# Optimization experiments

Measured on AMD Instinct MI355X. Metric: run time of the kernel, lower is better.

Reference implementation:

```python
import jax, jax.numpy as jnp
import numpy as np

B, H, W, C = 8, 64, 64, 768
NUM_HEADS = 12
KSIZE = 3
DILATIONS = (1, 2, 3)
ND = len(DILATIONS)
HEAD_DIM = C // NUM_HEADS  # 64
SCALE = HEAD_DIM ** (-0.5)


def setup_inputs() -> dict:
    key = jax.random.key(0)
    kx, kqkv, kpw, kpb = jax.random.split(key, 4)
    x = jax.random.normal(kx, (B, H, W, C), dtype=jnp.float32)
    # 1x1 conv qkv: weight [3C, C] (no bias, qkv_bias=False)
    qkv_w = jax.random.normal(kqkv, (3 * C, C), dtype=jnp.float32) * (C ** -0.5)
    # nn.Linear proj: weight [C, C], bias [C]
    proj_w = jax.random.normal(kpw, (C, C), dtype=jnp.float32) * (C ** -0.5)
    proj_b = jax.random.normal(kpb, (C,), dtype=jnp.float32) * 0.01
    return {"x": x, "qkv_w": qkv_w, "proj_w": proj_w, "proj_b": proj_b}


def _unfold(t, k, dil):
    # t: [B, d, H, W] -> [B, d, k*k, H, W]; matches nn.Unfold(k, dil, pad=dil*(k-1)//2)
    b, d, h, w = t.shape
    pad = dil * (k - 1) // 2
    tp = jnp.pad(t, ((0, 0), (0, 0), (pad, pad), (pad, pad)))
    patches = [tp[:, :, i * dil:i * dil + h, j * dil:j * dil + w]
               for i in range(k) for j in range(k)]
    return jnp.stack(patches, axis=2)


def reference(x, qkv_w, proj_w, proj_b):
    b, h, w, c = x.shape
    d = c // ND                 # channels per dilation group
    hpd = NUM_HEADS // ND       # heads per dilation group
    xc = x.transpose(0, 3, 1, 2)                      # [B, C, H, W]
    qkv = jnp.einsum('bchw,oc->bohw', xc, qkv_w)      # [B, 3C, H, W]
    qkv = qkv.reshape(b, 3, ND, d, h, w)
    outs = []
    for i, dil in enumerate(DILATIONS):
        q = qkv[:, 0, i].reshape(b, hpd, HEAD_DIM, h, w)
        ku = _unfold(qkv[:, 1, i], KSIZE, dil).reshape(b, hpd, HEAD_DIM, KSIZE * KSIZE, h, w)
        vu = _unfold(qkv[:, 2, i], KSIZE, dil).reshape(b, hpd, HEAD_DIM, KSIZE * KSIZE, h, w)
        attn = jnp.einsum('bnchw,bncKhw->bnKhw', q, ku) * SCALE
        attn = jax.nn.softmax(attn, axis=2)           # over the k*k neighborhood
        o = jnp.einsum('bnKhw,bncKhw->bnchw', attn, vu)  # [B, hpd, hd, H, W]
        outs.append(o.transpose(0, 3, 4, 1, 2).reshape(b, h, w, d))
    y = jnp.concatenate(outs, axis=-1)                # dilation-major channel order
    y = y + x                                          # DWConvAttention branch is identity
    y = jnp.einsum('bhwc,oc->bhwo', y, proj_w) + proj_b
    return y
```

## Files before the change

kernel.cpp:

```cpp
#include <hip/hip_runtime.h>
#include <hip/hip_bf16.h>

#define CC 768
#define MM 32768
#define NQKV 2304
#define SCALE_ 0.125f

typedef __bf16 bf16x8 __attribute__((ext_vector_type(8)));
typedef float f32x4 __attribute__((ext_vector_type(4)));
typedef unsigned short ushort8_t __attribute__((ext_vector_type(8)));

static __device__ __forceinline__ float bf2f(unsigned short u) {
  return __uint_as_float(((unsigned int)u) << 16);
}
static __device__ __forceinline__ unsigned short f2bf(float f) {
  __hip_bfloat16 t = __float2bfloat16(f);
  return __builtin_bit_cast(unsigned short, t);
}

__global__ void cvt_kernel(const float* __restrict__ in,
                           __hip_bfloat16* __restrict__ out, int n4) {
  int i = blockIdx.x * blockDim.x + threadIdx.x;
  if (i >= n4) return;
  float4 v = reinterpret_cast<const float4*>(in)[i];
  ushort4 o;
  o.x = f2bf(v.x); o.y = f2bf(v.y); o.z = f2bf(v.z); o.w = f2bf(v.w);
  reinterpret_cast<ushort4*>(out)[i] = o;
}

template <int MODE>
__global__ __launch_bounds__(256) void gemm_bf16_kernel(
    const __hip_bfloat16* __restrict__ A,
    const __hip_bfloat16* __restrict__ Bw,
    void* __restrict__ outp,
    const float* __restrict__ bias,
    int M, int N, int K) {
  __shared__ __hip_bfloat16 lA[3][128 * 32];
  __shared__ __hip_bfloat16 lB[3][128 * 32];

  const int nBN = N >> 7;
  const int cpx = gridDim.x >> 3;
  const int bid = ((int)blockIdx.x & 7) * cpx + ((int)blockIdx.x >> 3);
  const int bm = bid / nBN;
  const int bn = bid % nBN;
  const int tid = threadIdx.x;
  const int lane = tid & 63;
  const int wv = tid >> 6;
  const int wr = wv >> 1;
  const int wc = wv & 1;

  f32x4 acc[4][4] = {};

  const int srow = wv * 16 + (lane >> 2);
  const int scol = ((lane & 3) ^ ((lane >> 3) & 3)) * 8;
  const size_t Abase = (size_t)(bm * 128) * K;
  const size_t Bbase = (size_t)(bn * 128) * K;

  const int frow = lane & 15;
  const int g = lane >> 4;
  const int fcol = (g ^ ((frow >> 1) & 3)) * 8;

  auto stage = [&](int buf, int t) {
    const int k0 = t << 5;
#pragma unroll
    for (int c = 0; c < 2; ++c) {
      const __hip_bfloat16* gA = A + Abase + (size_t)(c * 64 + srow) * K + k0 + scol;
      __hip_bfloat16* sA = &lA[buf][(c * 64 + wv * 16) * 32];
      __builtin_amdgcn_global_load_lds(
          (const __attribute__((address_space(1))) void*)gA,
          (__attribute__((address_space(3))) void*)sA, 16, 0, 0);
      const __hip_bfloat16* gB = Bw + Bbase + (size_t)(c * 64 + srow) * K + k0 + scol;
      __hip_bfloat16* sB = &lB[buf][(c * 64 + wv * 16) * 32];
      __builtin_amdgcn_global_load_lds(
          (const __attribute__((address_space(1))) void*)gB,
          (__attribute__((address_space(3))) void*)sB, 16, 0, 0);
    }
  };

  const int nt = K >> 5;
  stage(0, 0);
  if (nt > 1) stage(1, 1);

  int rd = 0;
  int st = 2;
  for (int t = 0; t < nt; ++t) {
    if (t + 1 < nt) asm volatile("s_waitcnt vmcnt(4)" ::: "memory");
    else            asm volatile("s_waitcnt vmcnt(0)" ::: "memory");
    __builtin_amdgcn_s_barrier();
    asm volatile("" ::: "memory");

    bf16x8 af[4], bfr[4];
#pragma unroll
    for (int m = 0; m < 4; ++m)
      af[m] = *reinterpret_cast<const bf16x8*>(&lA[rd][(wr * 64 + m * 16 + frow) * 32 + fcol]);
#pragma unroll
    for (int n = 0; n < 4; ++n)
      bfr[n] = *reinterpret_cast<const bf16x8*>(&lB[rd][(wc * 64 + n * 16 + frow) * 32 + fcol]);

    if (t + 2 < nt) stage(st, t + 2);
#pragma unroll
    for (int m = 0; m < 4; ++m)
#pragma unroll
      for (int n = 0; n < 4; ++n)
        acc[m][n] = __builtin_amdgcn_mfma_f32_16x16x32_bf16(af[m], bfr[n], acc[m][n], 0, 0, 0);

    rd = (rd == 2) ? 0 : rd + 1;
    st = (st == 2) ? 0 : st + 1;
  }

  const int r0 = (lane >> 4) * 4;
  const int cc_ = lane & 15;
#pragma unroll
  for (int m = 0; m < 4; ++m) {
#pragma unroll
    for (int n = 0; n < 4; ++n) {
      const int grow = bm * 128 + wr * 64 + m * 16 + r0;
      const int gcol = bn * 128 + wc * 64 + n * 16 + cc_;
      if (MODE == 1) {
        __hip_bfloat16* outT = (__hip_bfloat16*)outp;
        ushort4 pk;
        pk.x = f2bf(acc[m][n][0]);
        pk.y = f2bf(acc[m][n][1]);
        pk.z = f2bf(acc[m][n][2]);
        pk.w = f2bf(acc[m][n][3]);
        *reinterpret_cast<ushort4*>(outT + (size_t)gcol * M + grow) = pk;
      } else {
        float* outF = (float*)outp;
        const float bv = bias ? bias[gcol] : 0.f;
#pragma unroll
        for (int r = 0; r < 4; ++r)
          outF[(size_t)(grow + r) * N + gcol] = acc[m][n][r] + bv;
      }
    }
  }
}

__global__ __launch_bounds__(256) void attn_kernel(
    const unsigned short* __restrict__ qkvT,
    const float* __restrict__ x,
    unsigned short* __restrict__ y) {
  const int head = blockIdx.x >> 7;
  const int p = ((blockIdx.x & 127) << 8) + threadIdx.x;
  const int h = (p >> 6) & 63;
  const int w = p & 63;
  const int grp = head >> 2;
  const int dil = grp + 1;
  const int chq = grp * 256 + (head & 3) * 64;

  int voff[9];
  bool valid[9];
#pragma unroll
  for (int t = 0; t < 9; ++t) {
    const int di = t / 3 - 1, dj = t % 3 - 1;
    valid[t] = ((unsigned)(h + di * dil) < 64u) && ((unsigned)(w + dj * dil) < 64u);
    voff[t] = p + (di * 64 + dj) * dil + 256;
  }
  const int voffq = p + 256;

  const unsigned short* qb = qkvT + (size_t)chq * MM - 256;
  const unsigned short* kb = qkvT + (size_t)(768 + chq) * MM - 256;

  float l[9] = {};
#pragma unroll 4
  for (int c = 0; c < 64; ++c) {
    const float qv = bf2f(qb[voffq]);
#pragma unroll
    for (int t = 0; t < 9; ++t)
      l[t] = fmaf(qv, bf2f(kb[voff[t]]), l[t]);
    qb += MM;
    kb += MM;
  }

#pragma unroll
  for (int t = 0; t < 9; ++t) l[t] = valid[t] ? l[t] * SCALE_ : 0.f;
  float mx = l[0];
#pragma unroll
  for (int t = 1; t < 9; ++t) mx = fmaxf(mx, l[t]);
  float den = 0.f;
#pragma unroll
  for (int t = 0; t < 9; ++t) {
    const float e = __expf(l[t] - mx);
    den += e;
    l[t] = valid[t] ? e : 0.f;
  }
  const float inv = 1.f / den;

  const unsigned short* vb = qkvT + (size_t)(1536 + chq) * MM - 256;
  float vout[64];
#pragma unroll
  for (int c = 0; c < 64; ++c) {
    float acc = 0.f;
#pragma unroll
    for (int t = 0; t < 9; ++t)
      acc = fmaf(l[t], bf2f(vb[voff[t]]), acc);
    vb += MM;
    vout[c] = acc * inv;
  }

  const float4* xr = reinterpret_cast<const float4*>(x + (size_t)p * CC + chq);
  ushort8_t* yr = reinterpret_cast<ushort8_t*>(y + (size_t)p * CC + chq);
#pragma unroll
  for (int k = 0; k < 8; ++k) {
    const float4 xa = xr[2 * k];
    const float4 xb4 = xr[2 * k + 1];
    ushort8_t o;
    o[0] = f2bf(vout[8 * k + 0] + xa.x);
    o[1] = f2bf(vout[8 * k + 1] + xa.y);
    o[2] = f2bf(vout[8 * k + 2] + xa.z);
    o[3] = f2bf(vout[8 * k + 3] + xa.w);
    o[4] = f2bf(vout[8 * k + 4] + xb4.x);
    o[5] = f2bf(vout[8 * k + 5] + xb4.y);
    o[6] = f2bf(vout[8 * k + 6] + xb4.z);
    o[7] = f2bf(vout[8 * k + 7] + xb4.w);
    yr[k] = o;
  }
}

extern "C" void kernel_launch(void* const* d_in, const int* in_sizes, int n_in,
                              void* d_out, int out_size, void* d_ws, size_t ws_size,
                              hipStream_t stream) {
  const float* x = (const float*)d_in[0];
  const float* qkv_w = (const float*)d_in[1];
  const float* proj_w = (const float*)d_in[2];
  const float* proj_b = (const float*)d_in[3];
  float* out = (float*)d_out;

  char* ws = (char*)d_ws;
  __hip_bfloat16* xb = (__hip_bfloat16*)(ws);
  __hip_bfloat16* qkvT = (__hip_bfloat16*)(ws + 50331648);
  __hip_bfloat16* wqkvb = (__hip_bfloat16*)(ws + 201326592);
  __hip_bfloat16* wprojb = (__hip_bfloat16*)(ws + 204865536);
  __hip_bfloat16* ybuf = xb;

  cvt_kernel<<<(MM * CC / 4 + 255) / 256, 256, 0, stream>>>(x, xb, MM * CC / 4);
  cvt_kernel<<<(NQKV * CC / 4 + 255) / 256, 256, 0, stream>>>(qkv_w, wqkvb, NQKV * CC / 4);
  cvt_kernel<<<(CC * CC / 4 + 255) / 256, 256, 0, stream>>>(proj_w, wprojb, CC * CC / 4);

  gemm_bf16_kernel<1><<<(MM / 128) * (NQKV / 128), 256, 0, stream>>>(
      xb, wqkvb, (void*)qkvT, nullptr, MM, NQKV, CC);

  attn_kernel<<<12 * 128, 256, 0, stream>>>(
      (const unsigned short*)qkvT, x, (unsigned short*)ybuf);

  gemm_bf16_kernel<2><<<(MM / 128) * (CC / 128), 256, 0, stream>>>(
      ybuf, wprojb, (void*)out, proj_b, MM, CC, CC);
}
```

Before: 417.1 us.

## Split attention channels across two blocks, batch loads, read bf16 residual

The attention kernel grid doubles so that each block computes only 32 of a head's 64 output channels. That cuts the register footprint, since the output buffer shrinks from 64 to 32 floats, and exposes more parallelism, but both halves recompute the full QK logits. The Q/K and V loops now issue groups of 4 channels × 9 taps of loads before doing the FMAs, to raise memory-level parallelism. The residual is read from the already-converted bf16 copy of x, which is aliased with the output buffer, instead of fp32 x. This halves residual traffic at some precision cost.

```diff
diff --git a/kernel.cpp b/kernel.cpp
--- a/kernel.cpp
+++ b/kernel.cpp
@@ -98,6 +98,7 @@
       bfr[n] = *reinterpret_cast<const bf16x8*>(&lB[rd][(wc * 64 + n * 16 + frow) * 32 + fcol]);
 
     if (t + 2 < nt) stage(st, t + 2);
+
 #pragma unroll
     for (int m = 0; m < 4; ++m)
 #pragma unroll
@@ -137,9 +138,11 @@
 
 __global__ __launch_bounds__(256) void attn_kernel(
     const unsigned short* __restrict__ qkvT,
-    const float* __restrict__ x,
+    const unsigned short* __restrict__ xres,
     unsigned short* __restrict__ y) {
-  const int head = blockIdx.x >> 7;
+  const int hh = blockIdx.x >> 7;
+  const int head = hh >> 1;
+  const int half = hh & 1;
   const int p = ((blockIdx.x & 127) << 8) + threadIdx.x;
   const int h = (p >> 6) & 63;
   const int w = p & 63;
@@ -161,14 +164,25 @@
   const unsigned short* kb = qkvT + (size_t)(768 + chq) * MM - 256;
 
   float l[9] = {};
-#pragma unroll 4
-  for (int c = 0; c < 64; ++c) {
-    const float qv = bf2f(qb[voffq]);
-#pragma unroll
-    for (int t = 0; t < 9; ++t)
-      l[t] = fmaf(qv, bf2f(kb[voff[t]]), l[t]);
-    qb += MM;
-    kb += MM;
+#pragma unroll 1
+  for (int cb = 0; cb < 16; ++cb) {
+    unsigned short qv[4];
+    unsigned short kv[4][9];
+#pragma unroll
+    for (int i = 0; i < 4; ++i) qv[i] = qb[voffq + i * MM];
+#pragma unroll
+    for (int i = 0; i < 4; ++i)
+#pragma unroll
+      for (int t = 0; t < 9; ++t) kv[i][t] = kb[voff[t] + i * MM];
+#pragma unroll
+    for (int i = 0; i < 4; ++i) {
+      const float qf = bf2f(qv[i]);
+#pragma unroll
+      for (int t = 0; t < 9; ++t)
+        l[t] = fmaf(qf, bf2f(kv[i][t]), l[t]);
+    }
+    qb += 4 * MM;
+    kb += 4 * MM;
   }
 
 #pragma unroll
@@ -184,34 +198,39 @@
     l[t] = valid[t] ? e : 0.f;
   }
   const float inv = 1.f / den;
-
-  const unsigned short* vb = qkvT + (size_t)(1536 + chq) * MM - 256;
-  float vout[64];
-#pragma unroll
-  for (int c = 0; c < 64; ++c) {
-    float acc = 0.f;
-#pragma unroll
-    for (int t = 0; t < 9; ++t)
-      acc = fmaf(l[t], bf2f(vb[voff[t]]), acc);
-    vb += MM;
-    vout[c] = acc * inv;
-  }
-
-  const float4* xr = reinterpret_cast<const float4*>(x + (size_t)p * CC + chq);
-  ushort8_t* yr = reinterpret_cast<ushort8_t*>(y + (size_t)p * CC + chq);
-#pragma unroll
-  for (int k = 0; k < 8; ++k) {
-    const float4 xa = xr[2 * k];
-    const float4 xb4 = xr[2 * k + 1];
+#pragma unroll
+  for (int t = 0; t < 9; ++t) l[t] *= inv;
+
+  const int cho = chq + half * 32;
+  const unsigned short* vb = qkvT + (size_t)(1536 + cho) * MM - 256;
+  float vout[32];
+#pragma unroll 1
+  for (int cb = 0; cb < 8; ++cb) {
+    unsigned short vv[4][9];
+#pragma unroll
+    for (int i = 0; i < 4; ++i)
+#pragma unroll
+      for (int t = 0; t < 9; ++t) vv[i][t] = vb[voff[t] + i * MM];
+#pragma unroll
+    for (int i = 0; i < 4; ++i) {
+      float acc = 0.f;
+#pragma unroll
+      for (int t = 0; t < 9; ++t)
+        acc = fmaf(l[t], bf2f(vv[i][t]), acc);
+      vout[cb * 4 + i] = acc;
+    }
+    vb += 4 * MM;
+  }
+
+  const ushort8_t* xr = reinterpret_cast<const ushort8_t*>(xres + (size_t)p * CC + cho);
+  ushort8_t* yr = reinterpret_cast<ushort8_t*>(y + (size_t)p * CC + cho);
+#pragma unroll
+  for (int k = 0; k < 4; ++k) {
+    const ushort8_t xa = xr[k];
     ushort8_t o;
-    o[0] = f2bf(vout[8 * k + 0] + xa.x);
-    o[1] = f2bf(vout[8 * k + 1] + xa.y);
-    o[2] = f2bf(vout[8 * k + 2] + xa.z);
-    o[3] = f2bf(vout[8 * k + 3] + xa.w);
-    o[4] = f2bf(vout[8 * k + 4] + xb4.x);
-    o[5] = f2bf(vout[8 * k + 5] + xb4.y);
-    o[6] = f2bf(vout[8 * k + 6] + xb4.z);
-    o[7] = f2bf(vout[8 * k + 7] + xb4.w);
+#pragma unroll
+    for (int j = 0; j < 8; ++j)
+      o[j] = f2bf(vout[8 * k + j] + bf2f(xa[j]));
     yr[k] = o;
   }
 }
@@ -239,8 +258,9 @@
   gemm_bf16_kernel<1><<<(MM / 128) * (NQKV / 128), 256, 0, stream>>>(
       xb, wqkvb, (void*)qkvT, nullptr, MM, NQKV, CC);
 
-  attn_kernel<<<12 * 128, 256, 0, stream>>>(
-      (const unsigned short*)qkvT, x, (unsigned short*)ybuf);
+  attn_kernel<<<24 * 128, 256, 0, stream>>>(
+      (const unsigned short*)qkvT, (const unsigned short*)xb,
+      (unsigned short*)ybuf);
 
   gemm_bf16_kernel<2><<<(MM / 128) * (CC / 128), 256, 0, stream>>>(
       ybuf, wprojb, (void*)out, proj_b, MM, CC, CC);
```

After: 385.7 us. 7.5% less time.
